# Performance work log

Hardware: AMD Instinct MI355X
Metric: run time of the kernel (lower is better)

Reference implementation:

```python
import jax, jax.numpy as jnp
import numpy as np

HEADS = 16
HEAD_DIM = 64
DIM = 1024
INNER = HEADS * HEAD_DIM
EPS = 1e-5


def setup_inputs() -> dict:
    key = jax.random.key(0)
    k_x, k_qkv, k_out, k_b = jax.random.split(key, 4)
    B, L = 2, 2048
    x = jax.random.normal(k_x, (B, L, DIM), dtype=jnp.float32)
    # Linear weights stored as [in, out] for x @ W
    w_qkv = jax.random.normal(k_qkv, (DIM, 3 * INNER), dtype=jnp.float32) * (DIM ** -0.5)
    w_out = jax.random.normal(k_out, (INNER, DIM), dtype=jnp.float32) * (INNER ** -0.5)
    b_out = jax.random.normal(k_b, (DIM,), dtype=jnp.float32) * 0.02
    gamma = jnp.ones((DIM,), dtype=jnp.float32)
    beta = jnp.zeros((DIM,), dtype=jnp.float32)
    return {"x": x, "w_qkv": w_qkv, "w_out": w_out, "b_out": b_out, "gamma": gamma, "beta": beta}


def reference(x, w_qkv, w_out, b_out, gamma, beta):
    B, L, C = x.shape
    scale = HEAD_DIM ** -0.5
    qkv = x @ w_qkv  # [B, L, 3*INNER]
    q, k, v = jnp.split(qkv, 3, axis=-1)
    # [B, L, INNER] -> [B, H, L, D]
    def split_heads(t):
        return t.reshape(B, L, HEADS, HEAD_DIM).transpose(0, 2, 1, 3)
    q, k, v = split_heads(q), split_heads(k), split_heads(v)
    dots = jnp.einsum('bhid,bhjd->bhij', q, k) * scale
    attn = jax.nn.softmax(dots, axis=-1)
    out = jnp.einsum('bhij,bhjd->bhid', attn, v)
    out = out.transpose(0, 2, 1, 3).reshape(B, L, INNER)
    out = out @ w_out + b_out
    res = x + out
    mean = jnp.mean(res, axis=-1, keepdims=True)
    var = jnp.var(res, axis=-1, keepdims=True)
    return (res - mean) * jax.lax.rsqrt(var + EPS) * gamma + beta
```

## Files before the change

### kernel.cpp

```cpp
#include <hip/hip_runtime.h>
#include <hip/hip_bf16.h>
#include <stdint.h>

#define HEADS 16
#define HDIM  64
#define DIMC  1024
#define INNER 1024
#define LSEQ  2048
#define BLM   4096

typedef unsigned short u16;
typedef __attribute__((ext_vector_type(8))) short bf16x8;
typedef __attribute__((ext_vector_type(4))) float f32x4;

__device__ __forceinline__ u16 f2bf(float f) {
  union { float f; uint32_t u; } v; v.f = f;
  uint32_t u = v.u;
  return (u16)((u + 0x7fffu + ((u >> 16) & 1u)) >> 16);
}
__device__ __forceinline__ uint32_t pack_bf2(float a, float b) {
  float2 f2; f2.x = a; f2.y = b;
  __hip_bfloat162 t = __float22bfloat162_rn(f2);
  union { __hip_bfloat162 h; uint32_t u; } c; c.h = t; return c.u;
}
__device__ __forceinline__ float fast_exp2(float x) {
  float r; asm("v_exp_f32 %0, %1" : "=v"(r) : "v"(x)); return r;
}

__device__ __forceinline__ void load_lds16(const void* g, void* l) {
  __builtin_amdgcn_global_load_lds(
      (const __attribute__((address_space(1))) uint32_t*)g,
      (__attribute__((address_space(3))) uint32_t*)l, 16, 0, 0);
}

__global__ __launch_bounds__(256) void cast_bf16_k(const float* __restrict__ in,
                                                   u16* __restrict__ out, int n) {
  int i = (blockIdx.x * 256 + threadIdx.x) * 4;
  if (i < n) {
    float4 v = *(const float4*)(in + i);
    ushort4 o;
    o.x = f2bf(v.x); o.y = f2bf(v.y); o.z = f2bf(v.z); o.w = f2bf(v.w);
    *(ushort4*)(out + i) = o;
  }
}

__global__ __launch_bounds__(256) void transpose_cast_k(const float* __restrict__ in,
                                                        u16* __restrict__ out,
                                                        int R, int C) {
  __shared__ float tile[32][33];
  int c0 = blockIdx.x * 32, r0 = blockIdx.y * 32;
  int j = threadIdx.x & 31, i0 = threadIdx.x >> 5;
#pragma unroll
  for (int p = 0; p < 4; ++p) {
    int i = i0 + p * 8;
    tile[i][j] = in[(size_t)(r0 + i) * C + (c0 + j)];
  }
  __syncthreads();
#pragma unroll
  for (int p = 0; p < 4; ++p) {
    int i = i0 + p * 8;
    out[(size_t)(c0 + i) * R + (r0 + j)] = f2bf(tile[j][i]);
  }
}

template <int EPI, int TM>
__global__ __launch_bounds__(256) void gemm_bt(const u16* __restrict__ A,
                                               const u16* __restrict__ Bt,
                                               u16* __restrict__ Cb,
                                               float* __restrict__ Cf,
                                               const float* __restrict__ bias,
                                               const float* __restrict__ resid,
                                               u16* __restrict__ Vt,
                                               int M, int N, int K) {
  constexpr int MI = TM / 32;
  __shared__ alignas(16) u16 As[TM * 64];
  __shared__ alignas(16) u16 Bs[128 * 64];
  const int tid = threadIdx.x;
  const int lane = tid & 63;
  const int w = tid >> 6;
  const int wm = w >> 1, wn = w & 1;
  const int m0 = blockIdx.y * TM, n0 = blockIdx.x * 128;
  const int ln = lane & 15, qq = lane >> 4;
  const f32x4 zero4 = {0.f, 0.f, 0.f, 0.f};

  f32x4 acc[MI][4];
#pragma unroll
  for (int i = 0; i < MI; ++i)
#pragma unroll
    for (int j = 0; j < 4; ++j) acc[i][j] = zero4;

  for (int kt = 0; kt < K; kt += 64) {
    __syncthreads();
#pragma unroll
    for (int p = 0; p < TM / 32; ++p) {
      int t = p * 256 + tid;
      int r = t >> 3;
      int cl = (t & 7) ^ (r & 7);
      load_lds16(A + (size_t)(m0 + r) * K + kt + cl * 8,
                 (char*)As + (p * 256 + w * 64) * 16);
    }
#pragma unroll
    for (int p = 0; p < 4; ++p) {
      int t = p * 256 + tid;
      int r = t >> 3;
      int cl = (t & 7) ^ (r & 7);
      load_lds16(Bt + (size_t)(n0 + r) * K + kt + cl * 8,
                 (char*)Bs + (p * 256 + w * 64) * 16);
    }
    __syncthreads();
#pragma unroll
    for (int ks = 0; ks < 2; ++ks) {
      bf16x8 af[MI], bfr[4];
#pragma unroll
      for (int i = 0; i < MI; ++i) {
        int ra = wm * (TM / 2) + i * 16 + ln;
        af[i] = *(const bf16x8*)(As + (ra * 8 + ((ks * 4 + qq) ^ (ra & 7))) * 8);
      }
#pragma unroll
      for (int j = 0; j < 4; ++j) {
        int rb = wn * 64 + j * 16 + ln;
        bfr[j] = *(const bf16x8*)(Bs + (rb * 8 + ((ks * 4 + qq) ^ (rb & 7))) * 8);
      }
#pragma unroll
      for (int i = 0; i < MI; ++i)
#pragma unroll
        for (int j = 0; j < 4; ++j)
          acc[i][j] = __builtin_amdgcn_mfma_f32_16x16x32_bf16(af[i], bfr[j],
                                                              acc[i][j], 0, 0, 0);
    }
  }

#pragma unroll
  for (int i = 0; i < MI; ++i) {
#pragma unroll
    for (int j = 0; j < 4; ++j) {
      int col = n0 + wn * 64 + j * 16 + ln;
      if (EPI == 1) {
#pragma unroll
        for (int rr = 0; rr < 4; ++rr) {
          int row = m0 + wm * (TM / 2) + i * 16 + qq * 4 + rr;
          Cf[(size_t)row * N + col] =
              acc[i][j][rr] + bias[col] + resid[(size_t)row * N + col];
        }
      } else {
        if (col < 2048) {
#pragma unroll
          for (int rr = 0; rr < 4; ++rr) {
            int row = m0 + wm * (TM / 2) + i * 16 + qq * 4 + rr;
            Cb[(size_t)row * 2048 + col] = f2bf(acc[i][j][rr]);
          }
        } else {
          int dg = col - 2048;
          int hh = dg >> 6, dd = dg & 63;
          int l0 = (m0 & 2047) + wm * (TM / 2) + i * 16 + qq * 4;
          int bb = m0 >> 11;
          ushort4 pk;
          pk.x = f2bf(acc[i][j][0]); pk.y = f2bf(acc[i][j][1]);
          pk.z = f2bf(acc[i][j][2]); pk.w = f2bf(acc[i][j][3]);
          *(ushort4*)(Vt + (((size_t)bb * 16 + hh) * 64 + dd) * 2048 + l0) = pk;
        }
      }
    }
  }
}

__global__ __launch_bounds__(256) void attn_fused(const u16* __restrict__ qk,
                                                  const u16* __restrict__ vt,
                                                  u16* __restrict__ outp) {
  const int qt = blockIdx.x & 31;
  const int h = (blockIdx.x >> 5) & 15;
  const int b = blockIdx.x >> 9;
  const int tid = threadIdx.x;
  const int lane = tid & 63;
  const int w = tid >> 6;
  const int ln = lane & 15, q4 = lane >> 4;
  const int l7 = ln & 7;
  const f32x4 zero4 = {0.f, 0.f, 0.f, 0.f};

  __shared__ alignas(16) u16 Ks[64 * 64];
  __shared__ alignas(16) u16 Vs[64 * 64];
  __shared__ alignas(16) u16 Ps[4][16 * 72];

  const size_t bh_tok = (size_t)b * LSEQ;
  const size_t vbase = ((size_t)b * 16 + h) * 64 * 2048;
  const int baseQ = h * HDIM;

  const float qscale = 0.125f * 1.44269504088896340736f;
  bf16x8 qf[2];
  {
    int row = qt * 64 + w * 16 + ln;
    const u16* p = qk + (bh_tok + row) * 2048 + baseQ;
#pragma unroll
    for (int ks = 0; ks < 2; ++ks) {
      bf16x8 v = *(const bf16x8*)(p + q4 * 8 + 32 * ks);
      bf16x8 o;
#pragma unroll
      for (int jj = 0; jj < 8; ++jj) {
        union { uint32_t u; float f; } cv; cv.u = ((uint32_t)(u16)v[jj]) << 16;
        o[jj] = (short)f2bf(cv.f * qscale);
      }
      qf[ks] = o;
    }
  }

  float lsum = 0.f;
  f32x4 o_acc[4];
#pragma unroll
  for (int dt = 0; dt < 4; ++dt) o_acc[dt] = zero4;

  u16* pw_base = &Ps[w][0];

  for (int jt = 0; jt < 32; ++jt) {
    const int key0 = jt * 64;
    __syncthreads();
#pragma unroll
    for (int iss = 0; iss < 2; ++iss) {
      int idx = iss * 256 + tid;
      int row = idx >> 3, c = idx & 7;
      int cl = c ^ (row & 7);
      load_lds16(qk + (bh_tok + key0 + row) * 2048 + 1024 + baseQ + cl * 8,
                 (char*)Ks + (iss * 256 + w * 64) * 16);
      load_lds16(vt + vbase + (size_t)row * 2048 + key0 + cl * 8,
                 (char*)Vs + (iss * 256 + w * 64) * 16);
    }
    __syncthreads();

    f32x4 S[4];
#pragma unroll
    for (int kt = 0; kt < 4; ++kt) {
      f32x4 a = zero4;
#pragma unroll
      for (int ks = 0; ks < 2; ++ks) {
        bf16x8 kf = *(const bf16x8*)(
            Ks + (((kt * 16 + ln) * 8 + ((ks * 4 + q4) ^ l7)) * 8));
        a = __builtin_amdgcn_mfma_f32_16x16x32_bf16(kf, qf[ks], a, 0, 0, 0);
      }
      S[kt] = a;
    }

#pragma unroll
    for (int kt = 0; kt < 4; ++kt)
#pragma unroll
      for (int r = 0; r < 4; ++r) {
        float p = fast_exp2(S[kt][r]);
        S[kt][r] = p;
        lsum += p;
      }

#pragma unroll
    for (int kt = 0; kt < 4; ++kt) {
      uint2 pd;
      pd.x = pack_bf2(S[kt][0], S[kt][1]);
      pd.y = pack_bf2(S[kt][2], S[kt][3]);
      *(uint2*)(pw_base + ln * 72 + kt * 16 + q4 * 4) = pd;
    }
    asm volatile("s_waitcnt lgkmcnt(0)" ::: "memory");

    bf16x8 pf0 = *(const bf16x8*)(pw_base + ln * 72 + 0 * 32 + q4 * 8);
    bf16x8 pf1 = *(const bf16x8*)(pw_base + ln * 72 + 1 * 32 + q4 * 8);

#pragma unroll
    for (int dt = 0; dt < 4; ++dt) {
      bf16x8 va0 = *(const bf16x8*)(
          Vs + (((dt * 16 + ln) * 8 + ((0 * 4 + q4) ^ l7)) * 8));
      o_acc[dt] = __builtin_amdgcn_mfma_f32_16x16x32_bf16(va0, pf0, o_acc[dt], 0, 0, 0);
      bf16x8 va1 = *(const bf16x8*)(
          Vs + (((dt * 16 + ln) * 8 + ((1 * 4 + q4) ^ l7)) * 8));
      o_acc[dt] = __builtin_amdgcn_mfma_f32_16x16x32_bf16(va1, pf1, o_acc[dt], 0, 0, 0);
    }
  }

  lsum += __shfl_xor(lsum, 16);
  lsum += __shfl_xor(lsum, 32);
  float rl = 1.0f / lsum;

  asm volatile("s_waitcnt lgkmcnt(0)" ::: "memory");
#pragma unroll
  for (int dt = 0; dt < 4; ++dt) {
    uint2 pd;
    pd.x = pack_bf2(o_acc[dt][0] * rl, o_acc[dt][1] * rl);
    pd.y = pack_bf2(o_acc[dt][2] * rl, o_acc[dt][3] * rl);
    *(uint2*)(pw_base + ln * 72 + dt * 16 + q4 * 4) = pd;
  }
  asm volatile("s_waitcnt lgkmcnt(0)" ::: "memory");
#pragma unroll
  for (int half = 0; half < 2; ++half) {
    int rr = half * 8 + (lane >> 3);
    int ch = lane & 7;
    bf16x8 rowv = *(const bf16x8*)(pw_base + rr * 72 + ch * 8);
    int tok = qt * 64 + w * 16 + rr;
    *(bf16x8*)(outp + (bh_tok + tok) * 1024 + baseQ + ch * 8) = rowv;
  }
}

__global__ __launch_bounds__(256) void ln_k(const float* __restrict__ res,
                                            const float* __restrict__ gamma,
                                            const float* __restrict__ beta,
                                            float* __restrict__ out) {
  int w = threadIdx.x >> 6, lane = threadIdx.x & 63;
  int row = blockIdx.x * 4 + w;
  const float* r = res + (size_t)row * DIMC;
  float4 v[4];
  float s = 0.f, ss = 0.f;
#pragma unroll
  for (int p = 0; p < 4; ++p) {
    v[p] = *(const float4*)(r + (p * 64 + lane) * 4);
    s += v[p].x + v[p].y + v[p].z + v[p].w;
    ss += v[p].x * v[p].x + v[p].y * v[p].y + v[p].z * v[p].z + v[p].w * v[p].w;
  }
#pragma unroll
  for (int off = 1; off < 64; off <<= 1) {
    s += __shfl_xor(s, off);
    ss += __shfl_xor(ss, off);
  }
  float mean = s * (1.0f / DIMC);
  float var = ss * (1.0f / DIMC) - mean * mean;
  float inv = rsqrtf(var + 1e-5f);
#pragma unroll
  for (int p = 0; p < 4; ++p) {
    int c = (p * 64 + lane) * 4;
    float4 g = *(const float4*)(gamma + c);
    float4 bt = *(const float4*)(beta + c);
    float4 o;
    o.x = (v[p].x - mean) * inv * g.x + bt.x;
    o.y = (v[p].y - mean) * inv * g.y + bt.y;
    o.z = (v[p].z - mean) * inv * g.z + bt.z;
    o.w = (v[p].w - mean) * inv * g.w + bt.w;
    *(float4*)(out + (size_t)row * DIMC + c) = o;
  }
}

extern "C" void kernel_launch(void* const* d_in, const int* in_sizes, int n_in,
                              void* d_out, int out_size, void* d_ws, size_t ws_size,
                              hipStream_t stream) {
  const float* x = (const float*)d_in[0];
  const float* w_qkv = (const float*)d_in[1];
  const float* w_out = (const float*)d_in[2];
  const float* b_out = (const float*)d_in[3];
  const float* gamma = (const float*)d_in[4];
  const float* beta = (const float*)d_in[5];
  float* outp = (float*)d_out;
  char* ws = (char*)d_ws;

  u16* xb = (u16*)(ws);
  u16* wqkvT = (u16*)(ws + ((size_t)8 << 20));
  u16* qk = (u16*)(ws + ((size_t)14 << 20));
  u16* vt = (u16*)(ws + ((size_t)30 << 20));
  u16* attnout = (u16*)(ws);
  u16* woutT = (u16*)(ws + ((size_t)8 << 20));
  float* res = (float*)(ws + ((size_t)14 << 20));

  cast_bf16_k<<<4096, 256, 0, stream>>>(x, xb, BLM * DIMC);
  transpose_cast_k<<<dim3(96, 32), 256, 0, stream>>>(w_qkv, wqkvT, 1024, 3072);
  gemm_bt<2, 128><<<dim3(24, 32), 256, 0, stream>>>(xb, wqkvT, qk, nullptr,
                                                    nullptr, nullptr, vt,
                                                    BLM, 3072, 1024);
  transpose_cast_k<<<dim3(32, 32), 256, 0, stream>>>(w_out, woutT, 1024, 1024);
  attn_fused<<<1024, 256, 0, stream>>>(qk, vt, attnout);
  gemm_bt<1, 64><<<dim3(8, 64), 256, 0, stream>>>(attnout, woutT, nullptr, res,
                                                  b_out, x, nullptr,
                                                  BLM, 1024, 1024);
  ln_k<<<1024, 256, 0, stream>>>(res, gamma, beta, outp);
}
```

Before: 204.6 us.

## Double-buffer K/V tiles in LDS and swizzle the P scratch buffer

The attention kernel now keeps two K/V LDS buffers and issues the global-to-LDS load of the next key tile before computing on the current one. This overlaps global memory latency with the MFMA and exp work, where before each tile was loaded and then waited on. The per-wave P/output scratch drops its 72-element padding in favour of a 64-wide XOR-swizzled layout to avoid LDS bank conflicts. The cost is twice the K/V LDS footprint, which may lower occupancy, plus slightly more index arithmetic.

```diff
diff --git a/kernel.cpp b/kernel.cpp
--- a/kernel.cpp
+++ b/kernel.cpp
@@ -177,9 +177,9 @@
   const int l7 = ln & 7;
   const f32x4 zero4 = {0.f, 0.f, 0.f, 0.f};
 
-  __shared__ alignas(16) u16 Ks[64 * 64];
-  __shared__ alignas(16) u16 Vs[64 * 64];
-  __shared__ alignas(16) u16 Ps[4][16 * 72];
+  __shared__ alignas(16) u16 Ks[2][64 * 64];
+  __shared__ alignas(16) u16 Vs[2][64 * 64];
+  __shared__ alignas(16) u16 Ps[4][16 * 64];
 
   const size_t bh_tok = (size_t)b * LSEQ;
   const size_t vbase = ((size_t)b * 16 + h) * 64 * 2048;
@@ -210,21 +210,20 @@
 
   u16* pw_base = &Ps[w][0];
 
-  for (int jt = 0; jt < 32; ++jt) {
-    const int key0 = jt * 64;
-    __syncthreads();
+  auto prefetch = [&](int key0, u16* Kd, u16* Vd) {
 #pragma unroll
     for (int iss = 0; iss < 2; ++iss) {
       int idx = iss * 256 + tid;
       int row = idx >> 3, c = idx & 7;
       int cl = c ^ (row & 7);
       load_lds16(qk + (bh_tok + key0 + row) * 2048 + 1024 + baseQ + cl * 8,
-                 (char*)Ks + (iss * 256 + w * 64) * 16);
+                 (char*)Kd + (iss * 256 + w * 64) * 16);
       load_lds16(vt + vbase + (size_t)row * 2048 + key0 + cl * 8,
-                 (char*)Vs + (iss * 256 + w * 64) * 16);
-    }
-    __syncthreads();
-
+                 (char*)Vd + (iss * 256 + w * 64) * 16);
+    }
+  };
+
+  auto compute = [&](const u16* Kc, const u16* Vc) {
     f32x4 S[4];
 #pragma unroll
     for (int kt = 0; kt < 4; ++kt) {
@@ -232,7 +231,7 @@
 #pragma unroll
       for (int ks = 0; ks < 2; ++ks) {
         bf16x8 kf = *(const bf16x8*)(
-            Ks + (((kt * 16 + ln) * 8 + ((ks * 4 + q4) ^ l7)) * 8));
+            Kc + (((kt * 16 + ln) * 8 + ((ks * 4 + q4) ^ l7)) * 8));
         a = __builtin_amdgcn_mfma_f32_16x16x32_bf16(kf, qf[ks], a, 0, 0, 0);
       }
       S[kt] = a;
@@ -252,22 +251,34 @@
       uint2 pd;
       pd.x = pack_bf2(S[kt][0], S[kt][1]);
       pd.y = pack_bf2(S[kt][2], S[kt][3]);
-      *(uint2*)(pw_base + ln * 72 + kt * 16 + q4 * 4) = pd;
+      int u = kt * 2 + (q4 >> 1);
+      *(uint2*)(pw_base + ln * 64 + ((u ^ l7) * 8) + (q4 & 1) * 4) = pd;
     }
     asm volatile("s_waitcnt lgkmcnt(0)" ::: "memory");
 
-    bf16x8 pf0 = *(const bf16x8*)(pw_base + ln * 72 + 0 * 32 + q4 * 8);
-    bf16x8 pf1 = *(const bf16x8*)(pw_base + ln * 72 + 1 * 32 + q4 * 8);
+    bf16x8 pf0 = *(const bf16x8*)(pw_base + ln * 64 + (((0 * 4 + q4) ^ l7) * 8));
+    bf16x8 pf1 = *(const bf16x8*)(pw_base + ln * 64 + (((1 * 4 + q4) ^ l7) * 8));
 
 #pragma unroll
     for (int dt = 0; dt < 4; ++dt) {
       bf16x8 va0 = *(const bf16x8*)(
-          Vs + (((dt * 16 + ln) * 8 + ((0 * 4 + q4) ^ l7)) * 8));
+          Vc + (((dt * 16 + ln) * 8 + ((0 * 4 + q4) ^ l7)) * 8));
       o_acc[dt] = __builtin_amdgcn_mfma_f32_16x16x32_bf16(va0, pf0, o_acc[dt], 0, 0, 0);
       bf16x8 va1 = *(const bf16x8*)(
-          Vs + (((dt * 16 + ln) * 8 + ((1 * 4 + q4) ^ l7)) * 8));
+          Vc + (((dt * 16 + ln) * 8 + ((1 * 4 + q4) ^ l7)) * 8));
       o_acc[dt] = __builtin_amdgcn_mfma_f32_16x16x32_bf16(va1, pf1, o_acc[dt], 0, 0, 0);
     }
+  };
+
+  prefetch(0, Ks[0], Vs[0]);
+
+  for (int jp = 0; jp < 16; ++jp) {
+    __syncthreads();
+    prefetch((2 * jp + 1) * 64, Ks[1], Vs[1]);
+    compute(Ks[0], Vs[0]);
+    __syncthreads();
+    if (jp < 15) prefetch((2 * jp + 2) * 64, Ks[0], Vs[0]);
+    compute(Ks[1], Vs[1]);
   }
 
   lsum += __shfl_xor(lsum, 16);
@@ -280,14 +291,15 @@
     uint2 pd;
     pd.x = pack_bf2(o_acc[dt][0] * rl, o_acc[dt][1] * rl);
     pd.y = pack_bf2(o_acc[dt][2] * rl, o_acc[dt][3] * rl);
-    *(uint2*)(pw_base + ln * 72 + dt * 16 + q4 * 4) = pd;
+    int u = dt * 2 + (q4 >> 1);
+    *(uint2*)(pw_base + ln * 64 + ((u ^ l7) * 8) + (q4 & 1) * 4) = pd;
   }
   asm volatile("s_waitcnt lgkmcnt(0)" ::: "memory");
 #pragma unroll
   for (int half = 0; half < 2; ++half) {
     int rr = half * 8 + (lane >> 3);
     int ch = lane & 7;
-    bf16x8 rowv = *(const bf16x8*)(pw_base + rr * 72 + ch * 8);
+    bf16x8 rowv = *(const bf16x8*)(pw_base + rr * 64 + ((ch ^ (rr & 7)) * 8));
     int tok = qt * 64 + w * 16 + rr;
     *(bf16x8*)(outp + (bh_tok + tok) * 1024 + baseQ + ch * 8) = rowv;
   }
```

After: 221.4 us. 8.2% more time.
